# Performance work log

Hardware: AMD Instinct MI355X
Metric: run time of the kernel (lower is better)

## Reference

```python
import jax, jax.numpy as jnp
import numpy as np

N = 100000      # nodes
E = 1600000     # edges (avg degree 16)
D_IN, D_H, D_OUT = 128, 128, 64


def setup_inputs() -> dict:
    key = jax.random.key(0)
    k1, k2, k3, k4 = jax.random.split(key, 4)
    x = jax.random.normal(k1, (N, D_IN), dtype=jnp.float32)
    edge_index = jax.random.randint(k2, (2, E), 0, N, dtype=jnp.int32)
    W1 = jax.random.normal(k3, (D_IN, D_H), dtype=jnp.float32) * (1.0 / np.sqrt(D_IN))
    b1 = jnp.zeros((D_H,), dtype=jnp.float32)
    W2 = jax.random.normal(k4, (D_H, D_OUT), dtype=jnp.float32) * (1.0 / np.sqrt(D_H))
    b2 = jnp.zeros((D_OUT,), dtype=jnp.float32)
    return {"x": x, "edge_index": edge_index, "W1": W1, "b1": b1, "W2": W2, "b2": b2}


def _gcn_conv(x, src, dst, W, b):
    """PyG GCNConv: out = D^{-1/2} (A + I) D^{-1/2} (x W) + b."""
    n = x.shape[0]
    h = x @ W  # [N, D_out] — transform first, then aggregate (PyG order)
    loops = jnp.arange(n, dtype=src.dtype)
    src_f = jnp.concatenate([src, loops])
    dst_f = jnp.concatenate([dst, loops])
    deg = jax.ops.segment_sum(jnp.ones_like(dst_f, dtype=h.dtype), dst_f, num_segments=n)
    dinv = jax.lax.rsqrt(deg)  # deg >= 1 due to self-loops
    norm = dinv[src_f] * dinv[dst_f]            # [E+N]
    msg = h[src_f] * norm[:, None]              # [E+N, D_out] gather
    out = jax.ops.segment_sum(msg, dst_f, num_segments=n)  # scatter-add
    return out + b


def reference(x, edge_index, W1, b1, W2, b2):
    src, dst = edge_index[0], edge_index[1]
    h = jax.nn.relu(_gcn_conv(x, src, dst, W1, b1))
    o = _gcn_conv(h, src, dst, W2, b2)
    return jax.nn.log_softmax(o, axis=1)
```

## Files before the change

kernel.cpp:

```cpp
#include <hip/hip_runtime.h>
#include <hip/hip_bf16.h>

typedef __hip_bfloat16 bf16;
typedef short short8 __attribute__((ext_vector_type(8)));
typedef float f32x4 __attribute__((ext_vector_type(4)));
typedef float f32x2 __attribute__((ext_vector_type(2)));

#define NPB 256
#define MAXBUK 1024

__device__ __forceinline__ float bf2f_raw(unsigned short u) {
    unsigned x = ((unsigned)u) << 16; float f; __builtin_memcpy(&f, &x, 4); return f;
}
__device__ __forceinline__ unsigned short f2bf_raw(float f) {
    unsigned u; __builtin_memcpy(&u, &f, 4);
    u += 0x7FFFu + ((u >> 16) & 1u);
    return (unsigned short)(u >> 16);
}
__device__ __forceinline__ float lo_f(unsigned u) {
    unsigned x = u << 16; float f; __builtin_memcpy(&f, &x, 4); return f;
}
__device__ __forceinline__ float hi_f(unsigned u) {
    unsigned x = u & 0xffff0000u; float f; __builtin_memcpy(&f, &x, 4); return f;
}


__global__ __launch_bounds__(256) void fatA_kernel(const unsigned short* __restrict__ W1s,
                                                   const void* __restrict__ W1p,
                                                   const void* __restrict__ W2p,
                                                   const void* __restrict__ b1p,
                                                   const void* __restrict__ b2p,
                                                   unsigned short* __restrict__ WB1,
                                                   unsigned short* __restrict__ WB2,
                                                   float* __restrict__ b1f,
                                                   float* __restrict__ b2f,
                                                   int* __restrict__ flag, int nshorts,
                                                   const int* __restrict__ dst,
                                                   int* __restrict__ bktcnt,
                                                   int E, int nbuk, int prepb) {
    __shared__ int smem[MAXBUK];
    const int tt = threadIdx.x;
    if ((int)blockIdx.x < prepb) {
        const int sample = min(nshorts, 2048);
        int c = 0;
        for (int i = tt; i < sample; i += 256) {
            unsigned e = (W1s[i] >> 7) & 0xFFu;
            if (e >= 140u || (e >= 1u && e <= 40u)) c++;
        }
        smem[tt] = c;
        __syncthreads();
        for (int o = 128; o > 0; o >>= 1) {
            if (tt < o) smem[tt] += smem[tt + o];
            __syncthreads();
        }
        const int isf32 = (smem[0] > sample / 8) ? 1 : 0;
        if (blockIdx.x == 0 && tt == 0) *flag = isf32;

        const int t = blockIdx.x * 256 + tt;
        const int T1 = 16384, T2 = 8192;
        if (t < T1) {
            int j = t & 7, l = (t >> 3) & 63, f = t >> 9;
            int n = f >> 2, kk = f & 3;
            int k = kk * 32 + (l >> 4) * 8 + j;
            int col = n * 16 + (l & 15);
            WB1[t] = isf32 ? f2bf_raw(((const float*)W1p)[k * 128 + col])
                           : ((const unsigned short*)W1p)[k * 128 + col];
        } else if (t < T1 + T2) {
            int o = t - T1;
            int j = o & 7, l = (o >> 3) & 63, f = o >> 9;
            int n = f >> 2, kk = f & 3;
            int k = kk * 32 + (l >> 4) * 8 + j;
            int col = n * 16 + (l & 15);
            WB2[o] = isf32 ? f2bf_raw(((const float*)W2p)[k * 64 + col])
                           : ((const unsigned short*)W2p)[k * 64 + col];
        } else if (t < T1 + T2 + 128) {
            int o = t - T1 - T2;
            b1f[o] = isf32 ? ((const float*)b1p)[o] : bf2f_raw(((const unsigned short*)b1p)[o]);
        } else if (t < T1 + T2 + 192) {
            int o = t - T1 - T2 - 128;
            b2f[o] = isf32 ? ((const float*)b2p)[o] : bf2f_raw(((const unsigned short*)b2p)[o]);
        }
    } else {
        const int e0 = ((int)blockIdx.x - prepb) * 4096;
        const int e1 = min(E, e0 + 4096);
        for (int b = tt; b < nbuk; b += 256) smem[b] = 0;
        __syncthreads();
        for (int e = e0 + tt; e < e1; e += 256) atomicAdd(&smem[dst[e] >> 8], 1);
        __syncthreads();
        for (int b = tt; b < nbuk; b += 256) {
            int c = smem[b];
            if (c) atomicAdd(&bktcnt[b], c);
        }
    }
}

__global__ __launch_bounds__(1024) void bscan_kernel(const int* __restrict__ bktcnt,
                                                     int* __restrict__ bofs,
                                                     int* __restrict__ bcur,
                                                     int nbuk, int total) {
    __shared__ int ps[1024];
    const int t = threadIdx.x;
    int v = (t < nbuk) ? bktcnt[t] : 0;
    ps[t] = v;
    __syncthreads();
    for (int o = 1; o < 1024; o <<= 1) {
        int u = (t >= o) ? ps[t - o] : 0;
        __syncthreads();
        ps[t] += u;
        __syncthreads();
    }
    if (t < nbuk) {
        int ex = ps[t] - v;
        bofs[t] = ex;
        bcur[t] = ex;
    }
    if (t == 0) bofs[nbuk] = total;
}

__global__ __launch_bounds__(256) void ms_scatter_kernel(const int* __restrict__ src,
                                                         const int* __restrict__ dst,
                                                         int* __restrict__ bcur,
                                                         unsigned* __restrict__ packed,
                                                         int E, int nbuk) {
    __shared__ int cnt[MAXBUK];
    __shared__ int gbase[MAXBUK];
    const int t = threadIdx.x;
    const int e0 = blockIdx.x * 4096;
    const int e1 = min(E, e0 + 4096);
    for (int b = t; b < nbuk; b += 256) cnt[b] = 0;
    __syncthreads();
    for (int e = e0 + t; e < e1; e += 256) atomicAdd(&cnt[dst[e] >> 8], 1);
    __syncthreads();
    for (int b = t; b < nbuk; b += 256) {
        int c = cnt[b];
        gbase[b] = c ? atomicAdd(&bcur[b], c) : 0;
        cnt[b] = 0;
    }
    __syncthreads();
    for (int e = e0 + t; e < e1; e += 256) {
        int d = dst[e];
        int b = d >> 8;
        int r = atomicAdd(&cnt[b], 1);
        packed[gbase[b] + r] = ((unsigned)(d & 255) << 24) | (unsigned)src[e];
    }
}

__global__ __launch_bounds__(256) void csr_fine2_kernel(const unsigned* __restrict__ packed,
                                                        const int* __restrict__ bofs,
                                                        uint2* __restrict__ nmeta,
                                                        float* __restrict__ dinv,
                                                        int* __restrict__ csrc, int n) {
    __shared__ int cnt2[NPB];
    __shared__ int cur[NPB];
    const int t = threadIdx.x;
    const int b = blockIdx.x;
    const int node0 = b << 8;
    const int nn = min(NPB, n - node0);
    cnt2[t] = 0;
    __syncthreads();
    const int beg = bofs[b], end = bofs[b + 1];
    for (int i = beg + t; i < end; i += 256) atomicAdd(&cnt2[packed[i] >> 24], 1);
    __syncthreads();
    int c = cnt2[t];
    cur[t] = c;
    __syncthreads();
    for (int o = 1; o < 256; o <<= 1) {
        int u = (t >= o) ? cur[t - o] : 0;
        __syncthreads();
        cur[t] += u;
        __syncthreads();
    }
    const int base = beg + cur[t] - c;
    if (t < nn) {
        nmeta[node0 + t] = make_uint2((unsigned)base, (unsigned)c);
        dinv[node0 + t] = rsqrtf((float)(c + 1));
    }
    __syncthreads();
    cur[t] = base;
    __syncthreads();
    for (int i = beg + t; i < end; i += 256) {
        unsigned u = packed[i];
        int pos = atomicAdd(&cur[u >> 24], 1);
        csrc[pos] = (int)(u & 0xFFFFFFu);
    }
}


__global__ __launch_bounds__(256) void gemm1p_mfma(const void* __restrict__ Xp,
                                                   const unsigned short* __restrict__ WB1,
                                                   const float* __restrict__ dinv,
                                                   unsigned char* __restrict__ Hf8, int nrows,
                                                   const int* __restrict__ flag) {
    __shared__ __align__(16) char smem[34816];
    unsigned short* Xs = (unsigned short*)smem;
    unsigned short* Cs = (unsigned short*)smem;
    const int t = threadIdx.x;
    const int r0 = blockIdx.x * 128;
    const int isf32 = *flag;

    if (isf32) {
        const float4* Xg = (const float4*)Xp;
        #pragma unroll
        for (int i = 0; i < 16; ++i) {
            int idx = t + 256 * i;
            int row = idx >> 5, c4 = idx & 31;
            float4 v = {0.f, 0.f, 0.f, 0.f};
            if (r0 + row < nrows) v = Xg[(size_t)(r0 + row) * 32 + c4];
            unsigned lo = (unsigned)f2bf_raw(v.x) | ((unsigned)f2bf_raw(v.y) << 16);
            unsigned hi = (unsigned)f2bf_raw(v.z) | ((unsigned)f2bf_raw(v.w) << 16);
            *reinterpret_cast<uint2*>(&Xs[row * 136 + c4 * 4]) = make_uint2(lo, hi);
        }
    } else {
        const uint4* Xg = (const uint4*)Xp;
        #pragma unroll
        for (int i = 0; i < 8; ++i) {
            int idx = t + 256 * i;
            int row = idx >> 4, c8 = idx & 15;
            uint4 v = {0u, 0u, 0u, 0u};
            if (r0 + row < nrows) v = Xg[(size_t)(r0 + row) * 16 + c8];
            *reinterpret_cast<uint4*>(&Xs[row * 136 + c8 * 8]) = v;
        }
    }
    __syncthreads();

    const int lane = t & 63, w = t >> 6;
    const int m0 = w * 32;
    short8 a[2][4];
    #pragma unroll
    for (int rt = 0; rt < 2; ++rt)
        #pragma unroll
        for (int kk = 0; kk < 4; ++kk)
            a[rt][kk] = *reinterpret_cast<const short8*>(
                &Xs[(m0 + rt * 16 + (lane & 15)) * 136 + kk * 32 + (lane >> 4) * 8]);
    __syncthreads();

    for (int p = 0; p < 2; ++p) {
        short8 b[4][4];
        #pragma unroll
        for (int n = 0; n < 4; ++n)
            #pragma unroll
            for (int kk = 0; kk < 4; ++kk)
                b[n][kk] = *reinterpret_cast<const short8*>(
                    WB1 + (size_t)(((p * 4 + n) * 4 + kk) * 64 + lane) * 8);
        f32x4 acc[2][4];
        #pragma unroll
        for (int rt = 0; rt < 2; ++rt)
            #pragma unroll
            for (int n = 0; n < 4; ++n) {
                acc[rt][n] = (f32x4){0.f, 0.f, 0.f, 0.f};
                #pragma unroll
                for (int kk = 0; kk < 4; ++kk)
                    acc[rt][n] = __builtin_amdgcn_mfma_f32_16x16x32_bf16(
                        a[rt][kk], b[n][kk], acc[rt][n], 0, 0, 0);
            }
        if (p) __syncthreads();
        #pragma unroll
        for (int rt = 0; rt < 2; ++rt)
            #pragma unroll
            for (int n = 0; n < 4; ++n)
                #pragma unroll
                for (int r = 0; r < 4; ++r) {
                    int row = m0 + rt * 16 + (lane >> 4) * 4 + r;
                    Cs[row * 68 + n * 16 + (lane & 15)] = f2bf_raw(acc[rt][n][r]);
                }
        __syncthreads();
        #pragma unroll
        for (int i = 0; i < 4; ++i) {
            int idx = t + 256 * i;
            int row = idx >> 3, c8 = idx & 7;
            if (r0 + row < nrows) {
                float dv = dinv[r0 + row];
                uint2 va = *reinterpret_cast<const uint2*>(&Cs[row * 68 + c8 * 8]);
                uint2 vb = *reinterpret_cast<const uint2*>(&Cs[row * 68 + c8 * 8 + 4]);
                int w0 = __builtin_amdgcn_cvt_pk_fp8_f32(dv * lo_f(va.x), dv * hi_f(va.x), 0, false);
                w0 = __builtin_amdgcn_cvt_pk_fp8_f32(dv * lo_f(va.y), dv * hi_f(va.y), w0, true);
                int w1 = __builtin_amdgcn_cvt_pk_fp8_f32(dv * lo_f(vb.x), dv * hi_f(vb.x), 0, false);
                w1 = __builtin_amdgcn_cvt_pk_fp8_f32(dv * lo_f(vb.y), dv * hi_f(vb.y), w1, true);
                *reinterpret_cast<uint2*>(Hf8 + (size_t)(r0 + row) * 128 + p * 64 + c8 * 8) =
                    make_uint2((unsigned)w0, (unsigned)w1);
            }
        }
        if (!p) __syncthreads();
    }
}


__device__ __forceinline__ void accf8_nw(f32x2* acc, uint2 v) {
    acc[0] += __builtin_amdgcn_cvt_pk_f32_fp8(v.x, false);
    acc[1] += __builtin_amdgcn_cvt_pk_f32_fp8(v.x, true);
    acc[2] += __builtin_amdgcn_cvt_pk_f32_fp8(v.y, false);
    acc[3] += __builtin_amdgcn_cvt_pk_f32_fp8(v.y, true);
}

__global__ __launch_bounds__(128) void agg128_v10(const uint2* __restrict__ H2,
                                                  const uint2* __restrict__ nmeta,
                                                  const int* __restrict__ csrc,
                                                  const float* __restrict__ biasf,
                                                  uint4* __restrict__ G4, int n) {
    const int lane = threadIdx.x & 63;
    const int g = lane >> 4;
    const int sub = lane & 15;
    const int node = blockIdx.x * 2 + (threadIdx.x >> 6);
    if (node >= n) return;

    uint2 vself = H2[((unsigned)node << 4) + (unsigned)sub];

    const uint2 meta = nmeta[node];
    const int base = (int)meta.x;
    const int cnt = (int)meta.y;
    const int end = base + cnt;
    const float di = rsqrtf((float)(cnt + 1));

    f32x2 acc[4];
    #pragma unroll
    for (int i = 0; i < 4; ++i) acc[i] = (f32x2){0.f, 0.f};
    if (g == 0) accf8_nw(acc, vself);

    int j = base;
    for (; j + 15 < end; j += 16) {
        int s0 = csrc[j + g];
        int s1 = csrc[j + 4 + g];
        int s2 = csrc[j + 8 + g];
        int s3 = csrc[j + 12 + g];
        uint2 v0 = H2[((unsigned)s0 << 4) + (unsigned)sub];
        uint2 v1 = H2[((unsigned)s1 << 4) + (unsigned)sub];
        uint2 v2 = H2[((unsigned)s2 << 4) + (unsigned)sub];
        uint2 v3 = H2[((unsigned)s3 << 4) + (unsigned)sub];
        accf8_nw(acc, v0);
        accf8_nw(acc, v1);
        accf8_nw(acc, v2);
        accf8_nw(acc, v3);
    }
    for (; j + 7 < end; j += 8) {
        int s0 = csrc[j + g];
        int s1 = csrc[j + 4 + g];
        uint2 v0 = H2[((unsigned)s0 << 4) + (unsigned)sub];
        uint2 v1 = H2[((unsigned)s1 << 4) + (unsigned)sub];
        accf8_nw(acc, v0);
        accf8_nw(acc, v1);
    }
    for (; j + 3 < end; j += 4) {
        int s0 = csrc[j + g];
        uint2 v0 = H2[((unsigned)s0 << 4) + (unsigned)sub];
        accf8_nw(acc, v0);
    }
    if (j + g < end) {
        int s0 = csrc[j + g];
        uint2 v0 = H2[((unsigned)s0 << 4) + (unsigned)sub];
        accf8_nw(acc, v0);
    }

    float a8[8];
    #pragma unroll
    for (int i = 0; i < 4; ++i) { a8[2 * i] = acc[i].x; a8[2 * i + 1] = acc[i].y; }
    #pragma unroll
    for (int i = 0; i < 8; ++i) {
        a8[i] += __shfl_xor(a8[i], 16, 64);
        a8[i] += __shfl_xor(a8[i], 32, 64);
    }

    if (g == 0) {
        const float4* b4 = (const float4*)biasf;
        float4 blo = b4[sub * 2], bhi = b4[sub * 2 + 1];
        a8[0] = fmaxf(fmaf(di, a8[0], blo.x), 0.f);
        a8[1] = fmaxf(fmaf(di, a8[1], blo.y), 0.f);
        a8[2] = fmaxf(fmaf(di, a8[2], blo.z), 0.f);
        a8[3] = fmaxf(fmaf(di, a8[3], blo.w), 0.f);
        a8[4] = fmaxf(fmaf(di, a8[4], bhi.x), 0.f);
        a8[5] = fmaxf(fmaf(di, a8[5], bhi.y), 0.f);
        a8[6] = fmaxf(fmaf(di, a8[6], bhi.z), 0.f);
        a8[7] = fmaxf(fmaf(di, a8[7], bhi.w), 0.f);
        uint4 o;
        o.x = (unsigned)f2bf_raw(a8[0]) | ((unsigned)f2bf_raw(a8[1]) << 16);
        o.y = (unsigned)f2bf_raw(a8[2]) | ((unsigned)f2bf_raw(a8[3]) << 16);
        o.z = (unsigned)f2bf_raw(a8[4]) | ((unsigned)f2bf_raw(a8[5]) << 16);
        o.w = (unsigned)f2bf_raw(a8[6]) | ((unsigned)f2bf_raw(a8[7]) << 16);
        G4[((unsigned)node << 4) + (unsigned)sub] = o;
    }
}


__global__ __launch_bounds__(256) void gemm2bp_mfma(const unsigned short* __restrict__ X,
                                                    const unsigned short* __restrict__ WB2,
                                                    const float* __restrict__ dinv,
                                                    unsigned short* __restrict__ T, int nrows) {
    __shared__ __align__(16) char smem[34816];
    unsigned short* Xs = (unsigned short*)smem;
    unsigned short* Cs = (unsigned short*)smem;
    const int t = threadIdx.x;
    const int r0 = blockIdx.x * 128;

    const uint4* Xg = (const uint4*)X;
    #pragma unroll
    for (int i = 0; i < 8; ++i) {
        int idx = t + 256 * i;
        int row = idx >> 4, c8 = idx & 15;
        uint4 v = {0u, 0u, 0u, 0u};
        if (r0 + row < nrows) v = Xg[(size_t)(r0 + row) * 16 + c8];
        *reinterpret_cast<uint4*>(&Xs[row * 136 + c8 * 8]) = v;
    }
    __syncthreads();

    const int lane = t & 63, w = t >> 6;
    const int m0 = w * 32;
    short8 a[2][4];
    #pragma unroll
    for (int rt = 0; rt < 2; ++rt)
        #pragma unroll
        for (int kk = 0; kk < 4; ++kk)
            a[rt][kk] = *reinterpret_cast<const short8*>(
                &Xs[(m0 + rt * 16 + (lane & 15)) * 136 + kk * 32 + (lane >> 4) * 8]);
    __syncthreads();

    short8 b[4][4];
    #pragma unroll
    for (int n = 0; n < 4; ++n)
        #pragma unroll
        for (int kk = 0; kk < 4; ++kk)
            b[n][kk] = *reinterpret_cast<const short8*>(
                WB2 + (size_t)((n * 4 + kk) * 64 + lane) * 8);

    f32x4 acc[2][4];
    #pragma unroll
    for (int rt = 0; rt < 2; ++rt)
        #pragma unroll
        for (int n = 0; n < 4; ++n) {
            acc[rt][n] = (f32x4){0.f, 0.f, 0.f, 0.f};
            #pragma unroll
            for (int kk = 0; kk < 4; ++kk)
                acc[rt][n] = __builtin_amdgcn_mfma_f32_16x16x32_bf16(
                    a[rt][kk], b[n][kk], acc[rt][n], 0, 0, 0);
        }

    #pragma unroll
    for (int rt = 0; rt < 2; ++rt)
        #pragma unroll
        for (int n = 0; n < 4; ++n)
            #pragma unroll
            for (int r = 0; r < 4; ++r) {
                int row = m0 + rt * 16 + (lane >> 4) * 4 + r;
                Cs[row * 68 + n * 16 + (lane & 15)] = f2bf_raw(acc[rt][n][r]);
            }
    __syncthreads();
    #pragma unroll
    for (int i = 0; i < 8; ++i) {
        int idx = t + 256 * i;
        int row = idx >> 4, c4 = idx & 15;
        if (r0 + row < nrows) {
            float dv = dinv[r0 + row];
            uint2 v = *reinterpret_cast<const uint2*>(&Cs[row * 68 + c4 * 4]);
            unsigned ox = (unsigned)f2bf_raw(dv * lo_f(v.x)) |
                          ((unsigned)f2bf_raw(dv * hi_f(v.x)) << 16);
            unsigned oy = (unsigned)f2bf_raw(dv * lo_f(v.y)) |
                          ((unsigned)f2bf_raw(dv * hi_f(v.y)) << 16);
            *reinterpret_cast<uint2*>(T + (size_t)(r0 + row) * 64 + c4 * 4) = make_uint2(ox, oy);
        }
    }
}


__device__ __forceinline__ void acc4v_nw(f32x2* acc, uint2 v) {
    acc[0] += (f32x2){lo_f(v.x), hi_f(v.x)};
    acc[1] += (f32x2){lo_f(v.y), hi_f(v.y)};
}

__global__ __launch_bounds__(128) void agg64_v3(const uint2* __restrict__ T2,
                                                const uint2* __restrict__ nmeta,
                                                const int* __restrict__ csrc,
                                                const float* __restrict__ b2f,
                                                void* __restrict__ OUTv, int n,
                                                const int* __restrict__ flag) {
    const int lane = threadIdx.x & 63;
    const int g = lane >> 4;
    const int sub = lane & 15;
    const int node = blockIdx.x * 2 + (threadIdx.x >> 6);
    if (node >= n) return;
    const int outf32 = *flag;

    uint2 vself = T2[((unsigned)node << 4) + (unsigned)sub];

    const uint2 meta = nmeta[node];
    const int base = (int)meta.x;
    const int cnt = (int)meta.y;
    const int end = base + cnt;
    const float di = rsqrtf((float)(cnt + 1));

    f32x2 acc[2];
    acc[0] = (f32x2){0.f, 0.f};
    acc[1] = (f32x2){0.f, 0.f};
    if (g == 0) acc4v_nw(acc, vself);

    int j = base;
    for (; j + 15 < end; j += 16) {
        int s0 = csrc[j + g];
        int s1 = csrc[j + 4 + g];
        int s2 = csrc[j + 8 + g];
        int s3 = csrc[j + 12 + g];
        uint2 v0 = T2[((unsigned)s0 << 4) + (unsigned)sub];
        uint2 v1 = T2[((unsigned)s1 << 4) + (unsigned)sub];
        uint2 v2 = T2[((unsigned)s2 << 4) + (unsigned)sub];
        uint2 v3 = T2[((unsigned)s3 << 4) + (unsigned)sub];
        acc4v_nw(acc, v0);
        acc4v_nw(acc, v1);
        acc4v_nw(acc, v2);
        acc4v_nw(acc, v3);
    }
    for (; j + 7 < end; j += 8) {
        int s0 = csrc[j + g];
        int s1 = csrc[j + 4 + g];
        uint2 v0 = T2[((unsigned)s0 << 4) + (unsigned)sub];
        uint2 v1 = T2[((unsigned)s1 << 4) + (unsigned)sub];
        acc4v_nw(acc, v0);
        acc4v_nw(acc, v1);
    }
    for (; j + 3 < end; j += 4) {
        int s0 = csrc[j + g];
        uint2 v0 = T2[((unsigned)s0 << 4) + (unsigned)sub];
        acc4v_nw(acc, v0);
    }
    if (j + g < end) {
        int s0 = csrc[j + g];
        uint2 v0 = T2[((unsigned)s0 << 4) + (unsigned)sub];
        acc4v_nw(acc, v0);
    }

    float a4[4] = {acc[0].x, acc[0].y, acc[1].x, acc[1].y};
    #pragma unroll
    for (int i = 0; i < 4; ++i) {
        a4[i] += __shfl_xor(a4[i], 16, 64);
        a4[i] += __shfl_xor(a4[i], 32, 64);
    }

    if (g == 0) {
        float4 bb = ((const float4*)b2f)[sub];
        a4[0] = fmaf(di, a4[0], bb.x);
        a4[1] = fmaf(di, a4[1], bb.y);
        a4[2] = fmaf(di, a4[2], bb.z);
        a4[3] = fmaf(di, a4[3], bb.w);

        float m = fmaxf(fmaxf(a4[0], a4[1]), fmaxf(a4[2], a4[3]));
        m = fmaxf(m, __shfl_xor(m, 1, 64));
        m = fmaxf(m, __shfl_xor(m, 2, 64));
        m = fmaxf(m, __shfl_xor(m, 4, 64));
        m = fmaxf(m, __shfl_xor(m, 8, 64));
        float s = __expf(a4[0] - m) + __expf(a4[1] - m) +
                  __expf(a4[2] - m) + __expf(a4[3] - m);
        s += __shfl_xor(s, 1, 64);
        s += __shfl_xor(s, 2, 64);
        s += __shfl_xor(s, 4, 64);
        s += __shfl_xor(s, 8, 64);
        const float lse = m + __logf(s);

        if (outf32) {
            float4 o = {a4[0] - lse, a4[1] - lse, a4[2] - lse, a4[3] - lse};
            ((float4*)OUTv)[(size_t)node * 16 + sub] = o;
        } else {
            uint2 o;
            o.x = (unsigned)f2bf_raw(a4[0] - lse) | ((unsigned)f2bf_raw(a4[1] - lse) << 16);
            o.y = (unsigned)f2bf_raw(a4[2] - lse) | ((unsigned)f2bf_raw(a4[3] - lse) << 16);
            ((uint2*)OUTv)[(size_t)node * 16 + sub] = o;
        }
    }
}


extern "C" void kernel_launch(void* const* d_in, const int* in_sizes, int n_in,
                              void* d_out, int out_size, void* d_ws, size_t ws_size,
                              hipStream_t stream) {
    const void* x  = d_in[0];
    const int*  ei = (const int*)d_in[1];
    const void* W1 = d_in[2];
    const void* b1 = d_in[3];
    const void* W2 = d_in[4];
    const void* b2 = d_in[5];

    const int N = in_sizes[0] / 128;
    const int E = in_sizes[1] / 2;
    const int* src = ei;
    const int* dst = ei + E;
    const int NBUK = (N + NPB - 1) / NPB;

    char* p = (char*)d_ws;
    auto alloc = [&](size_t bytes) { char* q = p; p += (bytes + 255) & ~255ull; return q; };
    int*   flag   = (int*)  alloc(4);
    uint2* nmeta  = (uint2*)alloc((size_t)N * 8);
    float* dinv   = (float*)alloc((size_t)N * 4);
    int*   bktcnt = (int*)  alloc((size_t)NBUK * 4);
    int*   bofs   = (int*)  alloc((size_t)(NBUK + 1) * 4);
    int*   bcur   = (int*)  alloc((size_t)NBUK * 4);
    float* b1f    = (float*)alloc(128 * 4);
    float* b2f    = (float*)alloc(64 * 4);
    unsigned short* WB1 = (unsigned short*)alloc(16384 * 2);
    unsigned short* WB2 = (unsigned short*)alloc(8192 * 2);
    unsigned* big = (unsigned*)alloc((size_t)N * 128 * 2);
    unsigned* packed = (unsigned*)d_out;
    int*      csrc   = (int*)d_in[1];
    unsigned* g1 = (unsigned*)d_in[0];
    unsigned short* T = (unsigned short*)big;
    (void)ws_size; (void)n_in; (void)out_size;

    const int PREPB = 97;
    const int MSB = (E + 4095) / 4096;
    const int GB = (N + 127) / 128;

    hipMemsetAsync(bktcnt, 0, (size_t)NBUK * 4, stream);
    fatA_kernel<<<PREPB + MSB, 256, 0, stream>>>((const unsigned short*)W1, W1, W2, b1, b2,
                                                 WB1, WB2, b1f, b2f, flag, in_sizes[2],
                                                 dst, bktcnt, E, NBUK, PREPB);
    bscan_kernel<<<1, 1024, 0, stream>>>(bktcnt, bofs, bcur, NBUK, E);
    ms_scatter_kernel<<<MSB, 256, 0, stream>>>(src, dst, bcur, packed, E, NBUK);
    csr_fine2_kernel<<<NBUK, 256, 0, stream>>>(packed, bofs, nmeta, dinv, csrc, N);

    gemm1p_mfma<<<GB, 256, 0, stream>>>(x, WB1, dinv, (unsigned char*)big, N, flag);
    agg128_v10<<<(N + 1) / 2, 128, 0, stream>>>((const uint2*)big, nmeta, csrc, b1f, (uint4*)g1, N);
    gemm2bp_mfma<<<GB, 256, 0, stream>>>((const unsigned short*)g1, WB2, dinv, T, N);
    agg64_v3<<<(N + 1) / 2, 128, 0, stream>>>((const uint2*)T, nmeta, csrc, b2f, d_out, N, flag);
}
```

Before: 280.7 us.

## Build CSR with per-node global atomics instead of two-level bucketed sort

The CSR build is restructured. Instead of bucket counts, a packed intermediate array and a fine per-bucket re-sort, degrees are counted per node with global atomics. Bucket offsets are derived from those degrees, a per-node prefix gives each node its base and cursor, and a single scatter pass places source indices using per-node atomic cursors. This drops one full pass over the packed edge array and the in-kernel LDS bucket histograms. In exchange it relies on many more random global atomics, and csrc moves into the spare half of the workspace buffer.

```diff
diff --git a/kernel.cpp b/kernel.cpp
--- a/kernel.cpp
+++ b/kernel.cpp
@@ -36,9 +36,9 @@
                                                    float* __restrict__ b2f,
                                                    int* __restrict__ flag, int nshorts,
                                                    const int* __restrict__ dst,
-                                                   int* __restrict__ bktcnt,
-                                                   int E, int nbuk, int prepb) {
-    __shared__ int smem[MAXBUK];
+                                                   int* __restrict__ deg,
+                                                   int E, int prepb) {
+    __shared__ int red[256];
     const int tt = threadIdx.x;
     if ((int)blockIdx.x < prepb) {
         const int sample = min(nshorts, 2048);
@@ -47,13 +47,13 @@
             unsigned e = (W1s[i] >> 7) & 0xFFu;
             if (e >= 140u || (e >= 1u && e <= 40u)) c++;
         }
-        smem[tt] = c;
+        red[tt] = c;
         __syncthreads();
         for (int o = 128; o > 0; o >>= 1) {
-            if (tt < o) smem[tt] += smem[tt + o];
+            if (tt < o) red[tt] += red[tt + o];
             __syncthreads();
         }
-        const int isf32 = (smem[0] > sample / 8) ? 1 : 0;
+        const int isf32 = (red[0] > sample / 8) ? 1 : 0;
         if (blockIdx.x == 0 && tt == 0) *flag = isf32;
 
         const int t = blockIdx.x * 256 + tt;
@@ -83,25 +83,32 @@
     } else {
         const int e0 = ((int)blockIdx.x - prepb) * 4096;
         const int e1 = min(E, e0 + 4096);
-        for (int b = tt; b < nbuk; b += 256) smem[b] = 0;
-        __syncthreads();
-        for (int e = e0 + tt; e < e1; e += 256) atomicAdd(&smem[dst[e] >> 8], 1);
-        __syncthreads();
-        for (int b = tt; b < nbuk; b += 256) {
-            int c = smem[b];
-            if (c) atomicAdd(&bktcnt[b], c);
-        }
-    }
-}
-
-__global__ __launch_bounds__(1024) void bscan_kernel(const int* __restrict__ bktcnt,
-                                                     int* __restrict__ bofs,
-                                                     int* __restrict__ bcur,
-                                                     int nbuk, int total) {
+        for (int e = e0 + tt; e < e1; e += 256) atomicAdd(&deg[dst[e]], 1);
+    }
+}
+
+__global__ __launch_bounds__(1024) void bscan2_kernel(const int* __restrict__ deg,
+                                                      int* __restrict__ bofs,
+                                                      int nbuk, int n, int total) {
     __shared__ int ps[1024];
     const int t = threadIdx.x;
-    int v = (t < nbuk) ? bktcnt[t] : 0;
-    ps[t] = v;
+    const int w = t >> 6, lane = t & 63;
+    ps[t] = 0;
+    __syncthreads();
+    for (int b = w; b < nbuk; b += 16) {
+        const int node0 = b << 8;
+        int s = 0;
+        #pragma unroll
+        for (int i = 0; i < 4; ++i) {
+            int idx = node0 + i * 64 + lane;
+            if (idx < n) s += deg[idx];
+        }
+        #pragma unroll
+        for (int o = 1; o < 64; o <<= 1) s += __shfl_xor(s, o, 64);
+        if (lane == 0) ps[b] = s;
+    }
+    __syncthreads();
+    int v = ps[t];
     __syncthreads();
     for (int o = 1; o < 1024; o <<= 1) {
         int u = (t >= o) ? ps[t - o] : 0;
@@ -109,79 +116,48 @@
         ps[t] += u;
         __syncthreads();
     }
-    if (t < nbuk) {
-        int ex = ps[t] - v;
-        bofs[t] = ex;
-        bcur[t] = ex;
-    }
+    if (t < nbuk) bofs[t] = ps[t] - v;
     if (t == 0) bofs[nbuk] = total;
 }
 
-__global__ __launch_bounds__(256) void ms_scatter_kernel(const int* __restrict__ src,
-                                                         const int* __restrict__ dst,
-                                                         int* __restrict__ bcur,
-                                                         unsigned* __restrict__ packed,
-                                                         int E, int nbuk) {
-    __shared__ int cnt[MAXBUK];
-    __shared__ int gbase[MAXBUK];
+__global__ __launch_bounds__(256) void fine3_kernel(const int* __restrict__ deg,
+                                                    const int* __restrict__ bofs,
+                                                    uint2* __restrict__ nmeta,
+                                                    float* __restrict__ dinv,
+                                                    int* __restrict__ cur, int n) {
+    __shared__ int sc[NPB];
+    const int t = threadIdx.x;
+    const int b = blockIdx.x;
+    const int node0 = b << 8;
+    const int node = node0 + t;
+    const int d = (node < n) ? deg[node] : 0;
+    sc[t] = d;
+    __syncthreads();
+    for (int o = 1; o < 256; o <<= 1) {
+        int u = (t >= o) ? sc[t - o] : 0;
+        __syncthreads();
+        sc[t] += u;
+        __syncthreads();
+    }
+    if (node < n) {
+        const int base = bofs[b] + sc[t] - d;
+        nmeta[node] = make_uint2((unsigned)base, (unsigned)d);
+        dinv[node] = rsqrtf((float)(d + 1));
+        cur[node] = base;
+    }
+}
+
+__global__ __launch_bounds__(256) void scatter3_kernel(const int* __restrict__ src,
+                                                       const int* __restrict__ dst,
+                                                       int* __restrict__ cur,
+                                                       int* __restrict__ csrc, int E) {
     const int t = threadIdx.x;
     const int e0 = blockIdx.x * 4096;
     const int e1 = min(E, e0 + 4096);
-    for (int b = t; b < nbuk; b += 256) cnt[b] = 0;
-    __syncthreads();
-    for (int e = e0 + t; e < e1; e += 256) atomicAdd(&cnt[dst[e] >> 8], 1);
-    __syncthreads();
-    for (int b = t; b < nbuk; b += 256) {
-        int c = cnt[b];
-        gbase[b] = c ? atomicAdd(&bcur[b], c) : 0;
-        cnt[b] = 0;
-    }
-    __syncthreads();
     for (int e = e0 + t; e < e1; e += 256) {
         int d = dst[e];
-        int b = d >> 8;
-        int r = atomicAdd(&cnt[b], 1);
-        packed[gbase[b] + r] = ((unsigned)(d & 255) << 24) | (unsigned)src[e];
-    }
-}
-
-__global__ __launch_bounds__(256) void csr_fine2_kernel(const unsigned* __restrict__ packed,
-                                                        const int* __restrict__ bofs,
-                                                        uint2* __restrict__ nmeta,
-                                                        float* __restrict__ dinv,
-                                                        int* __restrict__ csrc, int n) {
-    __shared__ int cnt2[NPB];
-    __shared__ int cur[NPB];
-    const int t = threadIdx.x;
-    const int b = blockIdx.x;
-    const int node0 = b << 8;
-    const int nn = min(NPB, n - node0);
-    cnt2[t] = 0;
-    __syncthreads();
-    const int beg = bofs[b], end = bofs[b + 1];
-    for (int i = beg + t; i < end; i += 256) atomicAdd(&cnt2[packed[i] >> 24], 1);
-    __syncthreads();
-    int c = cnt2[t];
-    cur[t] = c;
-    __syncthreads();
-    for (int o = 1; o < 256; o <<= 1) {
-        int u = (t >= o) ? cur[t - o] : 0;
-        __syncthreads();
-        cur[t] += u;
-        __syncthreads();
-    }
-    const int base = beg + cur[t] - c;
-    if (t < nn) {
-        nmeta[node0 + t] = make_uint2((unsigned)base, (unsigned)c);
-        dinv[node0 + t] = rsqrtf((float)(c + 1));
-    }
-    __syncthreads();
-    cur[t] = base;
-    __syncthreads();
-    for (int i = beg + t; i < end; i += 256) {
-        unsigned u = packed[i];
-        int pos = atomicAdd(&cur[u >> 24], 1);
-        csrc[pos] = (int)(u & 0xFFFFFFu);
+        int pos = atomicAdd(&cur[d], 1);
+        csrc[pos] = src[e];
     }
 }
 
@@ -585,16 +561,15 @@
     int*   flag   = (int*)  alloc(4);
     uint2* nmeta  = (uint2*)alloc((size_t)N * 8);
     float* dinv   = (float*)alloc((size_t)N * 4);
-    int*   bktcnt = (int*)  alloc((size_t)NBUK * 4);
+    int*   deg    = (int*)  alloc((size_t)N * 4);
+    int*   cur    = (int*)  alloc((size_t)N * 4);
     int*   bofs   = (int*)  alloc((size_t)(NBUK + 1) * 4);
-    int*   bcur   = (int*)  alloc((size_t)NBUK * 4);
     float* b1f    = (float*)alloc(128 * 4);
     float* b2f    = (float*)alloc(64 * 4);
     unsigned short* WB1 = (unsigned short*)alloc(16384 * 2);
     unsigned short* WB2 = (unsigned short*)alloc(8192 * 2);
     unsigned* big = (unsigned*)alloc((size_t)N * 128 * 2);
-    unsigned* packed = (unsigned*)d_out;
-    int*      csrc   = (int*)d_in[1];
+    int*      csrc = (int*)(big + (size_t)N * 32);
     unsigned* g1 = (unsigned*)d_in[0];
     unsigned short* T = (unsigned short*)big;
     (void)ws_size; (void)n_in; (void)out_size;
@@ -603,13 +578,13 @@
     const int MSB = (E + 4095) / 4096;
     const int GB = (N + 127) / 128;
 
-    hipMemsetAsync(bktcnt, 0, (size_t)NBUK * 4, stream);
+    hipMemsetAsync(deg, 0, (size_t)N * 4, stream);
     fatA_kernel<<<PREPB + MSB, 256, 0, stream>>>((const unsigned short*)W1, W1, W2, b1, b2,
                                                  WB1, WB2, b1f, b2f, flag, in_sizes[2],
-                                                 dst, bktcnt, E, NBUK, PREPB);
-    bscan_kernel<<<1, 1024, 0, stream>>>(bktcnt, bofs, bcur, NBUK, E);
-    ms_scatter_kernel<<<MSB, 256, 0, stream>>>(src, dst, bcur, packed, E, NBUK);
-    csr_fine2_kernel<<<NBUK, 256, 0, stream>>>(packed, bofs, nmeta, dinv, csrc, N);
+                                                 dst, deg, E, PREPB);
+    bscan2_kernel<<<1, 1024, 0, stream>>>(deg, bofs, NBUK, N, E);
+    fine3_kernel<<<NBUK, 256, 0, stream>>>(deg, bofs, nmeta, dinv, cur, N);
+    scatter3_kernel<<<MSB, 256, 0, stream>>>(src, dst, cur, csrc, E);
 
     gemm1p_mfma<<<GB, 256, 0, stream>>>(x, WB1, dinv, (unsigned char*)big, N, flag);
     agg128_v10<<<(N + 1) / 2, 128, 0, stream>>>((const uint2*)big, nmeta, csrc, b1f, (uint4*)g1, N);
```

Result: slower. 444.3 us (+58.3%).
